# Kernel tuning notes

Measured on AMD Instinct MI355X. Metric: run time of the kernel, lower is better.

The kernel has to match this reference:

```python
import jax, jax.numpy as jnp
import numpy as np

HID = 256
HEADS = 8
DPH = HID // HEADS  # 32
N = 65536
E = 262144


def _ln(x, g, b):
    m = jnp.mean(x, axis=-1, keepdims=True)
    v = jnp.var(x, axis=-1, keepdims=True)
    return (x - m) * jax.lax.rsqrt(v + 1e-5) * g + b


def _gelu(x):
    return jax.nn.gelu(x, approximate=False)


def _mlp2(x, W1, b1, W2, b2, act):
    return act(x @ W1 + b1) @ W2 + b2


def setup_inputs() -> dict:
    key = jax.random.key(0)
    ks = jax.random.split(key, 32)
    d = {}
    d["x"] = jax.random.normal(ks[0], (N, HID), jnp.float32)
    d["edge_index"] = jax.random.randint(ks[1], (2, E), 0, N, dtype=jnp.int32)
    d["edge_attr"] = jax.random.normal(ks[2], (E, 7), jnp.float32)
    i = 3
    def p(shape, s=0.02):
        nonlocal i
        out = jax.random.normal(ks[i], shape, jnp.float32) * s
        i += 1
        return out
    for nm, (din, dh, do) in [("q", (2 * HID + 3, 2 * HID, HID)),
                              ("k", (2 * HID + 3, 2 * HID, HID)),
                              ("v", (2 * HID + 3, 2 * HID, HID)),
                              ("s", (4, 64, HEADS)),
                              ("f", (HID, 2 * HID, HID))]:
        d[nm + "W1"] = p((din, dh))
        d[nm + "b1"] = jnp.zeros((dh,), jnp.float32)
        d[nm + "W2"] = p((dh, do))
        d[nm + "b2"] = jnp.zeros((do,), jnp.float32)
    d["ln_g"] = jnp.ones((HID,), jnp.float32)
    d["ln_b"] = jnp.zeros((HID,), jnp.float32)
    d["rW"] = p((2 * HID, HID))
    d["rb"] = jnp.zeros((HID,), jnp.float32)
    return d


def reference(x, edge_index, edge_attr,
              qW1, qb1, qW2, qb2,
              kW1, kb1, kW2, kb2,
              vW1, vb1, vW2, vb2,
              sW1, sb1, sW2, sb2,
              ln_g, ln_b, rW, rb,
              fW1, fb1, fW2, fb2):
    n_nodes = x.shape[0]
    original_x = x
    residual = x
    xn = _ln(x, ln_g, ln_b)

    src = edge_index[0]
    dst = edge_index[1]
    # gather endpoint features, concat with molecular edge feats -> [E, 2*HID+3]
    comb = jnp.concatenate([xn[src], xn[dst], edge_attr[:, :3]], axis=1)

    Q = _mlp2(comb, qW1, qb1, qW2, qb2, _gelu).reshape(-1, HEADS, DPH)
    K = _mlp2(comb, kW1, kb1, kW2, kb2, _gelu).reshape(-1, HEADS, DPH)
    V = _mlp2(comb, vW1, vb1, vW2, vb2, _gelu).reshape(-1, HEADS, DPH)

    scale = jnp.sqrt(jnp.float32(DPH))
    scores = jnp.einsum('ehd,egd->ehg', Q, K) / scale  # [E, H, H]
    bias = _mlp2(edge_attr[:, 3:7], sW1, sb1, sW2, sb2, jax.nn.relu)[:, :, None]  # [E, H, 1]
    attn = jax.nn.softmax(scores + bias, axis=1)  # softmax over dim=1, as in torch code
    wv = jnp.einsum('ehg,egd->ehd', attn, V).reshape(-1, HID)  # [E, HID]

    # scatter-mean to target nodes (edge_index[1])
    sums = jax.ops.segment_sum(wv, dst, num_segments=n_nodes)
    cnt = jax.ops.segment_sum(jnp.ones((wv.shape[0],), wv.dtype), dst, num_segments=n_nodes)
    out = sums / jnp.maximum(cnt, 1.0)[:, None]

    x1 = residual + out
    fused = jnp.concatenate([x1, original_x], axis=-1)
    x2 = x1 + (fused @ rW + rb)
    x3 = x2 + _mlp2(_ln(x2, ln_g, ln_b), fW1, fb1, fW2, fb2, _gelu)
    return x3
```

## Files before the change

kernel.cpp:

```cpp
#include <hip/hip_runtime.h>

#define N_NODES 65536
#define N_EDGES 262144
#define EBATCH 32768

typedef unsigned short u16;
typedef unsigned char u8;
typedef float f32x4 __attribute__((ext_vector_type(4)));
typedef _Float16 h2 __attribute__((ext_vector_type(2)));
typedef _Float16 v8h __attribute__((ext_vector_type(8)));

__device__ __forceinline__ u16 f2h(float f) {
  return __builtin_bit_cast(u16, (_Float16)f);
}
__device__ __forceinline__ u8 f2e5m2(float f) {
  _Float16 h = (_Float16)f;
  u16 hb = __builtin_bit_cast(u16, h);
  hb = (u16)(hb + 0x7F + ((hb >> 8) & 1));
  return (u8)(hb >> 8);
}
__device__ __forceinline__ void dec4(unsigned d, float* o) {
  o[0] = (float)__builtin_bit_cast(_Float16, (u16)((d << 8) & 0xFF00u));
  o[1] = (float)__builtin_bit_cast(_Float16, (u16)(d & 0xFF00u));
  o[2] = (float)__builtin_bit_cast(_Float16, (u16)((d >> 8) & 0xFF00u));
  o[3] = (float)__builtin_bit_cast(_Float16, (u16)((d >> 16) & 0xFF00u));
}
__device__ __forceinline__ h2 e5lo(unsigned d) {
  return __builtin_bit_cast(h2, __builtin_amdgcn_perm(d, 0u, 0x05000400u));
}
__device__ __forceinline__ h2 e5hi(unsigned d) {
  return __builtin_bit_cast(h2, __builtin_amdgcn_perm(d, 0u, 0x07000600u));
}
__device__ __forceinline__ float gelu_s(float x) {
  float e = __expf(1.702f * x);
  return x - __fdividef(x, e + 1.0f);
}
__device__ __forceinline__ float gelu_f(float x) {
  float y = 1.5957691216057308f * (x + 0.044715f * x * x * x);
  float e = __expf(y);
  return x - __fdividef(x, e + 1.0f);
}

__global__ __launch_bounds__(256) void ln_kernel(const float* __restrict__ x,
                                                 const float* __restrict__ g,
                                                 const float* __restrict__ b,
                                                 u16* __restrict__ out) {
  int row = blockIdx.x * 4 + (threadIdx.x >> 6);
  int lane = threadIdx.x & 63;
  float4 v = ((const float4*)(x + (size_t)row * 256))[lane];
  float s = v.x + v.y + v.z + v.w;
  float s2 = v.x * v.x + v.y * v.y + v.z * v.z + v.w * v.w;
#pragma unroll
  for (int off = 1; off < 64; off <<= 1) {
    s += __shfl_xor(s, off, 64);
    s2 += __shfl_xor(s2, off, 64);
  }
  float mean = s * (1.0f / 256.0f);
  float var = s2 * (1.0f / 256.0f) - mean * mean;
  float rs = rsqrtf(var + 1e-5f);
  float4 gv = ((const float4*)g)[lane];
  float4 bv = ((const float4*)b)[lane];
  ushort4 o;
  o.x = f2h((v.x - mean) * rs * gv.x + bv.x);
  o.y = f2h((v.y - mean) * rs * gv.y + bv.y);
  o.z = f2h((v.z - mean) * rs * gv.z + bv.z);
  o.w = f2h((v.w - mean) * rs * gv.w + bv.w);
  *(ushort4*)(out + (size_t)row * 256 + lane * 4) = o;
}

template <typename Epi>
__global__ __launch_bounds__(256) void gemm_bt(const u16* __restrict__ A,
                                               const u16* __restrict__ BT,
                                               int K, Epi epi) {
  __shared__ __align__(16) u16 sA[128 * 48];
  __shared__ __align__(16) u16 sB[128 * 48];
  const int tm = blockIdx.x * 128, tn = blockIdx.y * 128;
  const int t = threadIdx.x;
  const int wave = t >> 6, lane = t & 63;
  const int lrow = lane & 15, quad = lane >> 4;
  const int wrow = (wave & 1) * 64, wcol = (wave >> 1) * 64;
  const int r = t >> 2, c = (t & 3) << 3;
  f32x4 acc[4][4];
  const f32x4 z = {0.f, 0.f, 0.f, 0.f};
#pragma unroll
  for (int i = 0; i < 4; ++i)
#pragma unroll
    for (int j = 0; j < 4; ++j) acc[i][j] = z;
  for (int k0 = 0; k0 < K; k0 += 32) {
    *(uint4*)&sA[r * 48 + c] = *(const uint4*)&A[(size_t)(tm + r) * K + k0 + c];
    *(uint4*)&sA[(r + 64) * 48 + c] = *(const uint4*)&A[(size_t)(tm + r + 64) * K + k0 + c];
    *(uint4*)&sB[r * 48 + c] = *(const uint4*)&BT[(size_t)(tn + r) * K + k0 + c];
    *(uint4*)&sB[(r + 64) * 48 + c] = *(const uint4*)&BT[(size_t)(tn + r + 64) * K + k0 + c];
    __syncthreads();
    v8h af[4], bfv[4];
#pragma unroll
    for (int i = 0; i < 4; ++i) af[i] = *(const v8h*)&sA[(wrow + i * 16 + lrow) * 48 + quad * 8];
#pragma unroll
    for (int j = 0; j < 4; ++j) bfv[j] = *(const v8h*)&sB[(wcol + j * 16 + lrow) * 48 + quad * 8];
#pragma unroll
    for (int i = 0; i < 4; ++i)
#pragma unroll
      for (int j = 0; j < 4; ++j)
        acc[i][j] = __builtin_amdgcn_mfma_f32_16x16x32_f16(af[i], bfv[j], acc[i][j], 0, 0, 0);
    __syncthreads();
  }
#pragma unroll
  for (int i = 0; i < 4; ++i)
#pragma unroll
    for (int j = 0; j < 4; ++j)
#pragma unroll
      for (int rg = 0; rg < 4; ++rg)
        epi(tm + wrow + i * 16 + quad * 4 + rg, tn + wcol + j * 16 + lrow, acc[i][j][rg]);
}

struct EpiAB {
  u8* out;
  const float* b1cat;
  __device__ void operator()(int m, int n, float v) const {
    if (n < 1536) v += b1cat[n];
    out[(size_t)m * 3072 + n] = f2e5m2(v);
  }
};
struct EpiX2 {
  float* x2;
  const float* x1;
  const float* rb;
  __device__ void operator()(int m, int n, float v) const {
    x2[(size_t)m * 256 + n] = v + rb[n] + x1[(size_t)m * 256 + n];
  }
};
struct EpiHf {
  u16* hf;
  const float* b1;
  __device__ void operator()(int m, int n, float v) const {
    hf[(size_t)m * 512 + n] = f2h(gelu_f(v + b1[n]));
  }
};
struct EpiOut {
  float* out;
  const float* b2;
  const float* x2;
  __device__ void operator()(int m, int n, float v) const {
    out[(size_t)m * 256 + n] = v + b2[n] + x2[(size_t)m * 256 + n];
  }
};

__global__ void prep_w1catT(u16* __restrict__ out, const float* __restrict__ qW1,
                            const float* __restrict__ kW1, const float* __restrict__ vW1) {
  int cIdx = blockIdx.x;
  int rIdx = threadIdx.x;
  int sec = cIdx >> 9;
  int h = cIdx & 511;
  int mlp = sec % 3;
  const float* W1 = (mlp == 0) ? qW1 : (mlp == 1) ? kW1 : vW1;
  int rowoff = (sec < 3) ? 0 : 256;
  out[(size_t)cIdx * 256 + rIdx] = f2h(W1[(size_t)(rowoff + rIdx) * 512 + h]);
}
__global__ void prep_w2T(u16* __restrict__ out, const float* __restrict__ qW2,
                         const float* __restrict__ kW2, const float* __restrict__ vW2) {
  int row = blockIdx.x;
  int m = row >> 8, n = row & 255;
  const float* W2 = (m == 0) ? qW2 : (m == 1) ? kW2 : vW2;
  for (int k = threadIdx.x; k < 512; k += 256)
    out[(size_t)row * 512 + k] = f2h(W2[(size_t)k * 256 + n]);
}
__global__ void transpose_cast(u16* __restrict__ out, const float* __restrict__ in, int K, int Nn) {
  int n = blockIdx.x;
  for (int k = threadIdx.x; k < K; k += blockDim.x)
    out[(size_t)n * K + k] = f2h(in[(size_t)k * Nn + n]);
}
__global__ void prep_w1e16(u16* __restrict__ out, const float* __restrict__ qW1,
                           const float* __restrict__ kW1, const float* __restrict__ vW1) {
  int b = blockIdx.x;
  int m = b / 3, r = b % 3;
  const float* W1 = (m == 0) ? qW1 : (m == 1) ? kW1 : vW1;
  out[(size_t)b * 512 + threadIdx.x] = f2h(W1[(size_t)(512 + r) * 512 + threadIdx.x]);
}
__global__ void prep_b1cat(float* __restrict__ out, const float* __restrict__ qb1,
                           const float* __restrict__ kb1, const float* __restrict__ vb1) {
  int idx = blockIdx.x * 256 + threadIdx.x;
  const float* b = (idx < 512) ? qb1 : (idx < 1024) ? kb1 : vb1;
  out[idx] = b[idx & 511];
}

__global__ __launch_bounds__(256) void hist_kernel(const int* __restrict__ dst,
                                                   unsigned* __restrict__ cnt) {
  int e = blockIdx.x * 256 + threadIdx.x;
  atomicAdd(&cnt[dst[e]], 1u);
}
__global__ __launch_bounds__(1024) void scan_kernel(const unsigned* __restrict__ cnt,
                                                    unsigned* __restrict__ off,
                                                    unsigned* __restrict__ woff) {
  __shared__ unsigned s_part[1024];
  int t = threadIdx.x;
  unsigned local[64];
  unsigned run = 0;
  const uint4* cp = (const uint4*)(cnt + t * 64);
#pragma unroll
  for (int j = 0; j < 16; ++j) {
    uint4 v = cp[j];
    local[j * 4 + 0] = v.x; local[j * 4 + 1] = v.y;
    local[j * 4 + 2] = v.z; local[j * 4 + 3] = v.w;
  }
#pragma unroll
  for (int j = 0; j < 64; ++j) { unsigned c = local[j]; local[j] = run; run += c; }
  s_part[t] = run;
  __syncthreads();
  for (int d = 1; d < 1024; d <<= 1) {
    unsigned v = (t >= d) ? s_part[t - d] : 0u;
    __syncthreads();
    s_part[t] += v;
    __syncthreads();
  }
  unsigned base = (t == 0) ? 0u : s_part[t - 1];
  for (int j = 0; j < 64; ++j) {
    unsigned o = base + local[j];
    off[t * 64 + j] = o;
    woff[t * 64 + j] = o;
  }
}
__global__ __launch_bounds__(256) void scatter_ids(const int* __restrict__ dst,
                                                   unsigned* __restrict__ woff,
                                                   unsigned* __restrict__ eid) {
  int e = blockIdx.x * 256 + threadIdx.x;
  unsigned pos = atomicAdd(&woff[dst[e]], 1u);
  eid[pos] = (unsigned)e;
}

__global__ __launch_bounds__(256) void qkv_gemm(
    const int* __restrict__ eidx, const float* __restrict__ eattr,
    const u8* __restrict__ AB, const u16* __restrict__ W2T, const u16* __restrict__ w1e16,
    const float* __restrict__ qb2, const float* __restrict__ kb2, const float* __restrict__ vb2,
    int ebase, u8* __restrict__ qkv) {
  __shared__ __align__(16) u16 sH[64][136];
  __shared__ int s_src[64], s_dst[64];
  __shared__ __align__(16) float s_ea[64][4];
  const int m = blockIdx.y;
  const int t = threadIdx.x;
  const int e0 = ebase + blockIdx.x * 64;
  if (t < 64) {
    s_src[t] = eidx[e0 + t];
    s_dst[t] = eidx[N_EDGES + e0 + t];
  } else if (t >= 128 && t < 192) {
    int i = t - 128;
    const float* ea = eattr + (size_t)(e0 + i) * 7;
    s_ea[i][0] = ea[0]; s_ea[i][1] = ea[1]; s_ea[i][2] = ea[2];
  }
  __syncthreads();
  const int i = t & 63, seg = t >> 6;
  const int lane = t & 63, wave = t >> 6;
  const int lrow = lane & 15, quad = lane >> 4;
  const int wrow = (wave & 1) * 32, wcol = (wave >> 1) * 128;
  h2 ea0h, ea1h, ea2h;
  ea0h[0] = ea0h[1] = (_Float16)s_ea[i][0];
  ea1h[0] = ea1h[1] = (_Float16)s_ea[i][1];
  ea2h[0] = ea2h[1] = (_Float16)s_ea[i][2];
  const u8* rsB = AB + (size_t)s_src[i] * 3072 + m * 512 + seg * 32;
  const u8* rdB = AB + (size_t)s_dst[i] * 3072 + 1536 + m * 512 + seg * 32;
  const unsigned* w32 = (const unsigned*)(w1e16 + (size_t)m * 1536);
  f32x4 acc[2][8];
  const f32x4 z = {0.f, 0.f, 0.f, 0.f};
#pragma unroll
  for (int i2 = 0; i2 < 2; ++i2)
#pragma unroll
    for (int j = 0; j < 8; ++j) acc[i2][j] = z;
  for (int k0 = 0; k0 < 512; k0 += 128) {
    {
      alignas(16) unsigned sd[8], dd[8];
      *(uint4*)&sd[0] = *(const uint4*)(rsB + k0);
      *(uint4*)&sd[4] = *(const uint4*)(rsB + k0 + 16);
      *(uint4*)&dd[0] = *(const uint4*)(rdB + k0);
      *(uint4*)&dd[4] = *(const uint4*)(rdB + k0 + 16);
      const int cp0 = (k0 + seg * 32) >> 1;
      alignas(16) unsigned hout[16];
#pragma unroll
      for (int d = 0; d < 8; ++d) {
        int cp = cp0 + d * 2;
        h2 slo = e5lo(sd[d]) + e5lo(dd[d]);
        h2 shi = e5hi(sd[d]) + e5hi(dd[d]);
        slo += ea0h * __builtin_bit_cast(h2, w32[cp]);
        shi += ea0h * __builtin_bit_cast(h2, w32[cp + 1]);
        slo += ea1h * __builtin_bit_cast(h2, w32[256 + cp]);
        shi += ea1h * __builtin_bit_cast(h2, w32[256 + cp + 1]);
        slo += ea2h * __builtin_bit_cast(h2, w32[512 + cp]);
        shi += ea2h * __builtin_bit_cast(h2, w32[512 + cp + 1]);
        float g0 = gelu_s((float)slo[0]), g1 = gelu_s((float)slo[1]);
        float g2 = gelu_s((float)shi[0]), g3 = gelu_s((float)shi[1]);
        hout[d * 2] = (unsigned)f2h(g0) | ((unsigned)f2h(g1) << 16);
        hout[d * 2 + 1] = (unsigned)f2h(g2) | ((unsigned)f2h(g3) << 16);
      }
      uint4* hp = (uint4*)&sH[i][seg * 32];
      hp[0] = *(const uint4*)&hout[0];
      hp[1] = *(const uint4*)&hout[4];
      hp[2] = *(const uint4*)&hout[8];
      hp[3] = *(const uint4*)&hout[12];
    }
    __syncthreads();
#pragma unroll
    for (int ks = 0; ks < 4; ++ks) {
      int kk = ks * 32;
      v8h a0 = *(const v8h*)&sH[wrow + lrow][kk + quad * 8];
      v8h a1 = *(const v8h*)&sH[wrow + 16 + lrow][kk + quad * 8];
#pragma unroll
      for (int j = 0; j < 8; ++j) {
        v8h b = *(const v8h*)&W2T[(size_t)(m * 256 + wcol + j * 16 + lrow) * 512 + k0 + kk + quad * 8];
        acc[0][j] = __builtin_amdgcn_mfma_f32_16x16x32_f16(a0, b, acc[0][j], 0, 0, 0);
        acc[1][j] = __builtin_amdgcn_mfma_f32_16x16x32_f16(a1, b, acc[1][j], 0, 0, 0);
      }
    }
    __syncthreads();
  }
  const float* b2 = (m == 0) ? qb2 : (m == 1) ? kb2 : vb2;
  u8* sb = (u8*)sH;
#pragma unroll
  for (int i2 = 0; i2 < 2; ++i2)
#pragma unroll
    for (int j = 0; j < 8; ++j)
#pragma unroll
      for (int rg = 0; rg < 4; ++rg) {
        int row = wrow + i2 * 16 + quad * 4 + rg;
        int col = wcol + j * 16 + lrow;
        sb[row * 272 + col] = f2e5m2(acc[i2][j][rg] + b2[col]);
      }
  __syncthreads();
  {
    int ir = t >> 2, sg = t & 3;
    const u8* srcp = &sb[ir * 272 + sg * 64];
    uint4* dstp = (uint4*)(qkv + (size_t)(blockIdx.x * 64 + ir) * 768 + m * 256 + sg * 64);
    dstp[0] = *(const uint4*)srcp;
    dstp[1] = *(const uint4*)(srcp + 16);
    dstp[2] = *(const uint4*)(srcp + 32);
    dstp[3] = *(const uint4*)(srcp + 48);
  }
}

__global__ __launch_bounds__(256) void attn_kernel(
    const u8* __restrict__ qkv, const float* __restrict__ eattr,
    const float* __restrict__ sW1, const float* __restrict__ sb1,
    const float* __restrict__ sW2, const float* __restrict__ sb2,
    int ebase, u8* __restrict__ wv) {
  __shared__ __align__(16) u8 sQ[32][784];
  __shared__ float sS[32][8][8];
  const int t = threadIdx.x;
  const int el0 = blockIdx.x * 32;
  const int i = t >> 3, h = t & 7;
  {
    const uint4* g = (const uint4*)(qkv + (size_t)(el0 + i) * 768);
    uint4* l = (uint4*)&sQ[i][0];
#pragma unroll
    for (int j = 0; j < 6; ++j) l[h + j * 8] = g[h + j * 8];
  }
  float bias;
  {
    const float* ea = eattr + (size_t)(ebase + el0 + i) * 7;
    float a0 = ea[3], a1 = ea[4], a2 = ea[5], a3 = ea[6];
    float acc = sb2[h];
#pragma unroll 4
    for (int j = 0; j < 64; ++j) {
      float zz = fmaxf(a0 * sW1[j] + a1 * sW1[64 + j] + a2 * sW1[128 + j] + a3 * sW1[192 + j] + sb1[j], 0.f);
      acc += zz * sW2[j * 8 + h];
    }
    bias = acc;
  }
  __syncthreads();
  {
    alignas(16) unsigned qd[8];
    *(uint4*)&qd[0] = *(const uint4*)&sQ[i][h * 32];
    *(uint4*)&qd[4] = *(const uint4*)&sQ[i][h * 32 + 16];
    h2 qh[16];
#pragma unroll
    for (int d = 0; d < 8; ++d) { qh[d * 2] = e5lo(qd[d]); qh[d * 2 + 1] = e5hi(qd[d]); }
    float sc[8];
#pragma unroll
    for (int g = 0; g < 8; ++g) {
      alignas(16) unsigned kd[8];
      *(uint4*)&kd[0] = *(const uint4*)&sQ[i][256 + g * 32];
      *(uint4*)&kd[4] = *(const uint4*)&sQ[i][256 + g * 32 + 16];
      h2 acc;
      acc[0] = acc[1] = (_Float16)0.f;
#pragma unroll
      for (int d = 0; d < 8; ++d) {
        acc += qh[d * 2] * e5lo(kd[d]);
        acc += qh[d * 2 + 1] * e5hi(kd[d]);
      }
      sc[g] = (float)acc[0] + (float)acc[1];
    }
#pragma unroll
    for (int g = 0; g < 8; ++g) sS[i][h][g] = sc[g] * 0.17677669529663687f + bias;
  }
  __syncthreads();
  {
    int g = h;
    float mx = -1e30f;
#pragma unroll
    for (int hh = 0; hh < 8; ++hh) mx = fmaxf(mx, sS[i][hh][g]);
    float ev[8], ssum = 0.f;
#pragma unroll
    for (int hh = 0; hh < 8; ++hh) {
      ev[hh] = __expf(sS[i][hh][g] - mx);
      ssum += ev[hh];
    }
    float inv = 1.0f / ssum;
#pragma unroll
    for (int hh = 0; hh < 8; ++hh) sS[i][hh][g] = ev[hh] * inv;
  }
  __syncthreads();
  {
    h2 va[16];
#pragma unroll
    for (int u = 0; u < 16; ++u) va[u][0] = va[u][1] = (_Float16)0.f;
#pragma unroll
    for (int g = 0; g < 8; ++g) {
      float at = sS[i][h][g];
      h2 at2;
      at2[0] = at2[1] = (_Float16)at;
      alignas(16) unsigned vd[8];
      *(uint4*)&vd[0] = *(const uint4*)&sQ[i][512 + g * 32];
      *(uint4*)&vd[4] = *(const uint4*)&sQ[i][512 + g * 32 + 16];
#pragma unroll
      for (int d = 0; d < 8; ++d) {
        va[d * 2] += at2 * e5lo(vd[d]);
        va[d * 2 + 1] += at2 * e5hi(vd[d]);
      }
    }
    alignas(16) unsigned od[8];
#pragma unroll
    for (int p = 0; p < 8; ++p) {
      unsigned a = __builtin_bit_cast(unsigned, va[p * 2]) + 0x00800080u;
      unsigned b = __builtin_bit_cast(unsigned, va[p * 2 + 1]) + 0x00800080u;
      od[p] = __builtin_amdgcn_perm(b, a, 0x07050301u);
    }
    u8* dp = wv + (size_t)(ebase + el0 + i) * 256 + h * 32;
    *(uint4*)dp = *(const uint4*)&od[0];
    *(uint4*)(dp + 16) = *(const uint4*)&od[4];
  }
}

__global__ __launch_bounds__(256) void node_gather(const unsigned* __restrict__ off,
                                                   const unsigned* __restrict__ cnt,
                                                   const unsigned* __restrict__ eid,
                                                   const u8* __restrict__ wv,
                                                   const float* __restrict__ x,
                                                   float* __restrict__ x1,
                                                   u16* __restrict__ X1cat) {
  int n = blockIdx.x * 4 + (threadIdx.x >> 6);
  int lane = threadIdx.x & 63;
  unsigned st = off[n], c = cnt[n];
  float a0 = 0.f, a1 = 0.f, a2 = 0.f, a3 = 0.f;
  for (unsigned j = 0; j < c; ++j) {
    unsigned e = eid[st + j];
    unsigned d = *(const unsigned*)(wv + (size_t)e * 256 + lane * 4);
    float f[4];
    dec4(d, f);
    a0 += f[0]; a1 += f[1]; a2 += f[2]; a3 += f[3];
  }
  float inv = 1.0f / fmaxf((float)c, 1.0f);
  float4 xv = *(const float4*)(x + (size_t)n * 256 + lane * 4);
  float4 x1v = {xv.x + a0 * inv, xv.y + a1 * inv, xv.z + a2 * inv, xv.w + a3 * inv};
  *(float4*)(x1 + (size_t)n * 256 + lane * 4) = x1v;
  ushort4 a, bq;
  a.x = f2h(x1v.x); a.y = f2h(x1v.y); a.z = f2h(x1v.z); a.w = f2h(x1v.w);
  bq.x = f2h(xv.x); bq.y = f2h(xv.y); bq.z = f2h(xv.z); bq.w = f2h(xv.w);
  *(ushort4*)(X1cat + (size_t)n * 512 + lane * 4) = a;
  *(ushort4*)(X1cat + (size_t)n * 512 + 256 + lane * 4) = bq;
}

extern "C" void kernel_launch(void* const* d_in, const int* in_sizes, int n_in,
                              void* d_out, int out_size, void* d_ws, size_t ws_size,
                              hipStream_t stream) {
  const float* x = (const float*)d_in[0];
  const int* eidx = (const int*)d_in[1];
  const float* eattr = (const float*)d_in[2];
  const float* qW1 = (const float*)d_in[3];
  const float* qb1 = (const float*)d_in[4];
  const float* qW2 = (const float*)d_in[5];
  const float* qb2 = (const float*)d_in[6];
  const float* kW1 = (const float*)d_in[7];
  const float* kb1 = (const float*)d_in[8];
  const float* kW2 = (const float*)d_in[9];
  const float* kb2 = (const float*)d_in[10];
  const float* vW1 = (const float*)d_in[11];
  const float* vb1 = (const float*)d_in[12];
  const float* vW2 = (const float*)d_in[13];
  const float* vb2 = (const float*)d_in[14];
  const float* sW1 = (const float*)d_in[15];
  const float* sb1 = (const float*)d_in[16];
  const float* sW2 = (const float*)d_in[17];
  const float* sb2 = (const float*)d_in[18];
  const float* fW1 = (const float*)d_in[19];
  const float* fb1 = (const float*)d_in[20];
  const float* fW2 = (const float*)d_in[21];
  const float* fb2 = (const float*)d_in[22];
  const float* lng = (const float*)d_in[23];
  const float* lnb = (const float*)d_in[24];
  const float* rW = (const float*)d_in[25];
  const float* rb = (const float*)d_in[26];

  const size_t N = N_NODES;
  char* ws = (char*)d_ws;
  size_t off_b = 0;
  auto alloc = [&](size_t bytes) {
    void* p = ws + off_b;
    off_b = (off_b + bytes + 255) & ~(size_t)255;
    return p;
  };
  u16* W1catT = (u16*)alloc((size_t)3072 * 256 * 2);
  u16* W2T = (u16*)alloc((size_t)768 * 512 * 2);
  u16* rWT = (u16*)alloc((size_t)256 * 512 * 2);
  u16* fW1T = (u16*)alloc((size_t)512 * 256 * 2);
  u16* fW2T = (u16*)alloc((size_t)256 * 512 * 2);
  u16* w1e16 = (u16*)alloc((size_t)9 * 512 * 2);
  float* b1cat = (float*)alloc((size_t)1536 * 4);
  unsigned* cnt = (unsigned*)alloc(N * 4);
  unsigned* offs = (unsigned*)alloc(N * 4);
  unsigned* woff = (unsigned*)alloc(N * 4);
  unsigned* eid = (unsigned*)alloc((size_t)N_EDGES * 4);
  u8* qkv = (u8*)alloc((size_t)EBATCH * 768);
  u8* AB = (u8*)alloc(N * 3072);
  u16* xn = (u16*)d_out;
  u8* wv = (u8*)d_out;
  float* x1 = (float*)AB;
  u16* X1cat = (u16*)(AB + (size_t)67108864);
  float* x2 = (float*)(AB + (size_t)134217728);
  u16* xn2 = (u16*)AB;
  u16* Hf = (u16*)(AB + (size_t)33554432);

  hipMemsetAsync(cnt, 0, N * 4, stream);
  hist_kernel<<<N_EDGES / 256, 256, 0, stream>>>(eidx + N_EDGES, cnt);
  scan_kernel<<<1, 1024, 0, stream>>>(cnt, offs, woff);
  scatter_ids<<<N_EDGES / 256, 256, 0, stream>>>(eidx + N_EDGES, woff, eid);
  prep_w1catT<<<3072, 256, 0, stream>>>(W1catT, qW1, kW1, vW1);
  prep_w2T<<<768, 256, 0, stream>>>(W2T, qW2, kW2, vW2);
  prep_w1e16<<<9, 512, 0, stream>>>(w1e16, qW1, kW1, vW1);
  prep_b1cat<<<6, 256, 0, stream>>>(b1cat, qb1, kb1, vb1);
  transpose_cast<<<256, 256, 0, stream>>>(rWT, rW, 512, 256);
  transpose_cast<<<512, 256, 0, stream>>>(fW1T, fW1, 256, 512);
  transpose_cast<<<256, 256, 0, stream>>>(fW2T, fW2, 512, 256);

  ln_kernel<<<N_NODES / 4, 256, 0, stream>>>(x, lng, lnb, xn);
  gemm_bt<<<dim3(N_NODES / 128, 3072 / 128), 256, 0, stream>>>(xn, W1catT, 256, EpiAB{AB, b1cat});
  for (int b = 0; b < N_EDGES / EBATCH; ++b) {
    int ebase = b * EBATCH;
    qkv_gemm<<<dim3(EBATCH / 64, 3), 256, 0, stream>>>(eidx, eattr, AB, W2T, w1e16,
                                                       qb2, kb2, vb2, ebase, qkv);
    attn_kernel<<<EBATCH / 32, 256, 0, stream>>>(qkv, eattr, sW1, sb1, sW2, sb2, ebase, wv);
  }
  node_gather<<<N_NODES / 4, 256, 0, stream>>>(offs, cnt, eid, wv, x, x1, X1cat);
  gemm_bt<<<dim3(N_NODES / 128, 2), 256, 0, stream>>>(X1cat, rWT, 512, EpiX2{x2, x1, rb});
  ln_kernel<<<N_NODES / 4, 256, 0, stream>>>(x2, lng, lnb, xn2);
  gemm_bt<<<dim3(N_NODES / 128, 4), 256, 0, stream>>>(xn2, fW1T, 256, EpiHf{Hf, fb1});
  gemm_bt<<<dim3(N_NODES / 128, 2), 256, 0, stream>>>(Hf, fW2T, 512, EpiOut{(float*)d_out, fb2, x2});
}
```

Baseline: 1.978 ms.

## Use direct global-to-LDS loads in GEMMs and stage AB epilogue through LDS

Replaces the register-staged GEMM tile loads with global_load_lds 16-byte direct copies into an MFMA-fragment-ordered LDS layout, so the fragment reads become contiguous per lane. The large node GEMM producing the fp8 AB buffer now writes its output tile into LDS first and stores coalesced 16-byte rows, instead of scattered byte stores. It also uses a 1D grid with a swizzled block order that spreads M tiles across groups to improve cache locality. The loop is still single-buffered, and the new LDS layout relies on the direct-to-LDS lane ordering matching the fragment order.

```diff
diff --git a/kernel.cpp b/kernel.cpp
--- a/kernel.cpp
+++ b/kernel.cpp
@@ -39,6 +39,11 @@
   float y = 1.5957691216057308f * (x + 0.044715f * x * x * x);
   float e = __expf(y);
   return x - __fdividef(x, e + 1.0f);
+}
+__device__ __forceinline__ void gld16(const u16* g, u16* l) {
+  __builtin_amdgcn_global_load_lds(
+      (const __attribute__((address_space(1))) void*)g,
+      (__attribute__((address_space(3))) void*)l, 16, 0, 0);
 }
 
 __global__ __launch_bounds__(256) void ln_kernel(const float* __restrict__ x,
@@ -68,42 +73,56 @@
   *(ushort4*)(out + (size_t)row * 256 + lane * 4) = o;
 }
 
+#define GEMM_CORE(K_)                                                                   \
+  const int t = threadIdx.x;                                                            \
+  const int wave = t >> 6, lane = t & 63;                                               \
+  const int lrow = lane & 15, quad = lane >> 4;                                         \
+  const int wrow = (wave & 1) * 64, wcol = (wave >> 1) * 64;                            \
+  const int sa0 = 2 * wave, sa1 = 2 * wave + 1;                                         \
+  const u16* pa0 = A + (size_t)(tm + sa0 * 16 + lrow) * (K_) + quad * 8;                \
+  const u16* pa1 = A + (size_t)(tm + sa1 * 16 + lrow) * (K_) + quad * 8;                \
+  const u16* pb0 = BT + (size_t)(tn + sa0 * 16 + lrow) * (K_) + quad * 8;               \
+  const u16* pb1 = BT + (size_t)(tn + sa1 * 16 + lrow) * (K_) + quad * 8;               \
+  u16* la0 = &sAB[sa0 * 512];                                                           \
+  u16* la1 = &sAB[sa1 * 512];                                                           \
+  u16* lb0 = &sAB[4096 + sa0 * 512];                                                    \
+  u16* lb1 = &sAB[4096 + sa1 * 512];                                                    \
+  f32x4 acc[4][4];                                                                      \
+  {                                                                                     \
+    const f32x4 z = {0.f, 0.f, 0.f, 0.f};                                               \
+    _Pragma("unroll") for (int i = 0; i < 4; ++i)                                       \
+        _Pragma("unroll") for (int j = 0; j < 4; ++j) acc[i][j] = z;                    \
+  }                                                                                     \
+  for (int k0 = 0; k0 < (K_); k0 += 32) {                                               \
+    gld16(pa0, la0);                                                                    \
+    gld16(pa1, la1);                                                                    \
+    gld16(pb0, lb0);                                                                    \
+    gld16(pb1, lb1);                                                                    \
+    pa0 += 32;                                                                          \
+    pa1 += 32;                                                                          \
+    pb0 += 32;                                                                          \
+    pb1 += 32;                                                                          \
+    __syncthreads();                                                                    \
+    v8h af[4], bfv[4];                                                                  \
+    _Pragma("unroll") for (int i = 0; i < 4; ++i) af[i] =                               \
+        *(const v8h*)&sAB[((wave & 1) * 4 + i) * 512 + lane * 8];                       \
+    _Pragma("unroll") for (int j = 0; j < 4; ++j) bfv[j] =                              \
+        *(const v8h*)&sAB[4096 + ((wave >> 1) * 4 + j) * 512 + lane * 8];               \
+    _Pragma("unroll") for (int i = 0; i < 4; ++i)                                       \
+        _Pragma("unroll") for (int j = 0; j < 4; ++j) acc[i][j] =                       \
+            __builtin_amdgcn_mfma_f32_16x16x32_f16(af[i], bfv[j], acc[i][j], 0, 0, 0);  \
+    __syncthreads();                                                                    \
+  }
+
 template <typename Epi>
-__global__ __launch_bounds__(256) void gemm_bt(const u16* __restrict__ A,
-                                               const u16* __restrict__ BT,
-                                               int K, Epi epi) {
-  __shared__ __align__(16) u16 sA[128 * 48];
-  __shared__ __align__(16) u16 sB[128 * 48];
-  const int tm = blockIdx.x * 128, tn = blockIdx.y * 128;
-  const int t = threadIdx.x;
-  const int wave = t >> 6, lane = t & 63;
-  const int lrow = lane & 15, quad = lane >> 4;
-  const int wrow = (wave & 1) * 64, wcol = (wave >> 1) * 64;
-  const int r = t >> 2, c = (t & 3) << 3;
-  f32x4 acc[4][4];
-  const f32x4 z = {0.f, 0.f, 0.f, 0.f};
-#pragma unroll
-  for (int i = 0; i < 4; ++i)
-#pragma unroll
-    for (int j = 0; j < 4; ++j) acc[i][j] = z;
-  for (int k0 = 0; k0 < K; k0 += 32) {
-    *(uint4*)&sA[r * 48 + c] = *(const uint4*)&A[(size_t)(tm + r) * K + k0 + c];
-    *(uint4*)&sA[(r + 64) * 48 + c] = *(const uint4*)&A[(size_t)(tm + r + 64) * K + k0 + c];
-    *(uint4*)&sB[r * 48 + c] = *(const uint4*)&BT[(size_t)(tn + r) * K + k0 + c];
-    *(uint4*)&sB[(r + 64) * 48 + c] = *(const uint4*)&BT[(size_t)(tn + r + 64) * K + k0 + c];
-    __syncthreads();
-    v8h af[4], bfv[4];
-#pragma unroll
-    for (int i = 0; i < 4; ++i) af[i] = *(const v8h*)&sA[(wrow + i * 16 + lrow) * 48 + quad * 8];
-#pragma unroll
-    for (int j = 0; j < 4; ++j) bfv[j] = *(const v8h*)&sB[(wcol + j * 16 + lrow) * 48 + quad * 8];
-#pragma unroll
-    for (int i = 0; i < 4; ++i)
-#pragma unroll
-      for (int j = 0; j < 4; ++j)
-        acc[i][j] = __builtin_amdgcn_mfma_f32_16x16x32_f16(af[i], bfv[j], acc[i][j], 0, 0, 0);
-    __syncthreads();
-  }
+__global__ __launch_bounds__(256) void gemm2(const u16* __restrict__ A,
+                                             const u16* __restrict__ BT,
+                                             int K, int NT, Epi epi) {
+  __shared__ __align__(16) u16 sAB[8192];
+  const int bid = blockIdx.x;
+  const int mt = bid / NT, nt = bid % NT;
+  const int tm = mt * 128, tn = nt * 128;
+  GEMM_CORE(K)
 #pragma unroll
   for (int i = 0; i < 4; ++i)
 #pragma unroll
@@ -113,14 +132,42 @@
         epi(tm + wrow + i * 16 + quad * 4 + rg, tn + wcol + j * 16 + lrow, acc[i][j][rg]);
 }
 
-struct EpiAB {
-  u8* out;
-  const float* b1cat;
-  __device__ void operator()(int m, int n, float v) const {
-    if (n < 1536) v += b1cat[n];
-    out[(size_t)m * 3072 + n] = f2e5m2(v);
-  }
-};
+__global__ __launch_bounds__(256) void gemm2_ab(const u16* __restrict__ A,
+                                                const u16* __restrict__ BT,
+                                                const float* __restrict__ b1cat,
+                                                u8* __restrict__ out) {
+  __shared__ __align__(16) u16 sAB[8192];
+  const int bid = blockIdx.x;
+  const int local = bid >> 3;
+  const int mt = (bid & 7) * 64 + local / 24;
+  const int nt = local % 24;
+  const int tm = mt * 128, tn = nt * 128;
+  GEMM_CORE(256)
+  float bj[4];
+#pragma unroll
+  for (int j = 0; j < 4; ++j)
+    bj[j] = (nt < 12) ? b1cat[tn + wcol + j * 16 + lrow] : 0.f;
+  u8* sb = (u8*)sAB;
+#pragma unroll
+  for (int i = 0; i < 4; ++i)
+#pragma unroll
+    for (int j = 0; j < 4; ++j)
+#pragma unroll
+      for (int rg = 0; rg < 4; ++rg)
+        sb[(wrow + i * 16 + quad * 4 + rg) * 128 + wcol + j * 16 + lrow] =
+            f2e5m2(acc[i][j][rg] + bj[j]);
+  __syncthreads();
+  {
+    int r = t >> 1, half = t & 1;
+    const uint4* sp = (const uint4*)&sb[r * 128 + half * 64];
+    uint4* dp = (uint4*)(out + (size_t)(tm + r) * 3072 + tn + half * 64);
+    dp[0] = sp[0];
+    dp[1] = sp[1];
+    dp[2] = sp[2];
+    dp[3] = sp[3];
+  }
+}
+
 struct EpiX2 {
   float* x2;
   const float* x1;
@@ -538,7 +585,7 @@
   transpose_cast<<<256, 256, 0, stream>>>(fW2T, fW2, 512, 256);
 
   ln_kernel<<<N_NODES / 4, 256, 0, stream>>>(x, lng, lnb, xn);
-  gemm_bt<<<dim3(N_NODES / 128, 3072 / 128), 256, 0, stream>>>(xn, W1catT, 256, EpiAB{AB, b1cat});
+  gemm2_ab<<<12288, 256, 0, stream>>>(xn, W1catT, b1cat, AB);
   for (int b = 0; b < N_EDGES / EBATCH; ++b) {
     int ebase = b * EBATCH;
     qkv_gemm<<<dim3(EBATCH / 64, 3), 256, 0, stream>>>(eidx, eattr, AB, W2T, w1e16,
@@ -546,8 +593,8 @@
     attn_kernel<<<EBATCH / 32, 256, 0, stream>>>(qkv, eattr, sW1, sb1, sW2, sb2, ebase, wv);
   }
   node_gather<<<N_NODES / 4, 256, 0, stream>>>(offs, cnt, eid, wv, x, x1, X1cat);
-  gemm_bt<<<dim3(N_NODES / 128, 2), 256, 0, stream>>>(X1cat, rWT, 512, EpiX2{x2, x1, rb});
+  gemm2<<<N_NODES / 128 * 2, 256, 0, stream>>>(X1cat, rWT, 512, 2, EpiX2{x2, x1, rb});
   ln_kernel<<<N_NODES / 4, 256, 0, stream>>>(x2, lng, lnb, xn2);
-  gemm_bt<<<dim3(N_NODES / 128, 4), 256, 0, stream>>>(xn2, fW1T, 256, EpiHf{Hf, fb1});
-  gemm_bt<<<dim3(N_NODES / 128, 2), 256, 0, stream>>>(Hf, fW2T, 512, EpiOut{(float*)d_out, fb2, x2});
-}
+  gemm2<<<N_NODES / 128 * 4, 256, 0, stream>>>(xn2, fW1T, 256, 4, EpiHf{Hf, fb1});
+  gemm2<<<N_NODES / 128 * 2, 256, 0, stream>>>(Hf, fW2T, 512, 2, EpiOut{(float*)d_out, fb2, x2});
+}
```

New measurement: 1.980 ms. Within noise of the previous version (+0.1%).
